# Kernel optimization log

Measured on AMD Instinct MI355X. Metric: run time of the kernel, lower is better.

Reference implementation:

```python
import jax, jax.numpy as jnp
import numpy as np

BETA = 0.25
EPS = 1e-12  # torch F.normalize eps


def _normalize(x):
    n = jnp.linalg.norm(x, axis=-1, keepdims=True)
    return x / jnp.maximum(n, EPS)


def setup_inputs() -> dict:
    key = jax.random.key(0)
    k1, k2 = jax.random.split(key)
    B, S, D, NE = 16, 2048, 512, 8192
    z = jax.random.normal(k1, (B, S, D), dtype=jnp.float32)
    emb = jax.random.normal(k2, (NE, D), dtype=jnp.float32)
    return {"z": z, "emb": emb}


def reference(z, emb):
    B, S, D = z.shape
    n_e = emb.shape[0]
    zf = z.reshape(-1, D)                      # [N, D]
    zn = _normalize(zf)
    embn = _normalize(emb)                     # [n_e, D]
    # squared euclidean distances: [N, n_e]
    d = (jnp.sum(zn * zn, axis=1, keepdims=True)
         + jnp.sum(embn * embn, axis=1)
         - 2.0 * jnp.matmul(zn, embn.T))
    idx = jnp.argmin(d, axis=1)                # [N]
    z_q = emb[idx].reshape(z.shape)            # raw codebook lookup (NOT normalized)
    # commitment / codebook loss on normalized vectors
    z_q_n = _normalize(z_q)
    z_n = _normalize(z)
    sg = jax.lax.stop_gradient
    loss = (jnp.mean((z_q_n - sg(z_n)) ** 2)
            + BETA * jnp.mean((sg(z_q_n) - z_n) ** 2))
    # straight-through estimator, then normalize
    z_q_st = z + sg(z_q - z)
    z_q_st = _normalize(z_q_st)
    # perplexity via usage counts (equivalent to mean of one-hots)
    N = zf.shape[0]
    counts = jnp.zeros((n_e,), dtype=z.dtype).at[idx].add(1.0)
    e_mean = counts / N
    perplexity = jnp.exp(-jnp.sum(e_mean * jnp.log(e_mean + 1e-10)))
    return loss, z_q_st, idx, perplexity
```

## Files before the change

### kernel.cpp

```cpp
#include <hip/hip_runtime.h>
#include <float.h>
#include <math.h>

#define DIM 512
#define EPSN 1e-12f

typedef _Float16 f16x8 __attribute__((ext_vector_type(8)));
typedef float f32x4 __attribute__((ext_vector_type(4)));

__device__ inline void gll16(const void* g, void* l) {
  __builtin_amdgcn_global_load_lds(
      (__attribute__((address_space(1))) void*)g,
      (__attribute__((address_space(3))) void*)l, 16, 0, 0);
}

__device__ inline float wave_sum(float v) {
#pragma unroll
  for (int o = 32; o > 0; o >>= 1) v += __shfl_xor(v, o, 64);
  return v;
}

__global__ __launch_bounds__(256) void emb_norm_kernel(
    const float* __restrict__ emb, float2* __restrict__ eepair) {
  int row = blockIdx.x * 4 + (threadIdx.x >> 6);
  int lane = threadIdx.x & 63;
  const float* p = emb + (size_t)row * DIM;
  float x[8];
  float ss = 0.f;
#pragma unroll
  for (int i = 0; i < 8; ++i) { x[i] = p[i * 64 + lane]; ss += x[i] * x[i]; }
  ss = wave_sum(ss);
  float d = fmaxf(sqrtf(ss), EPSN);
  float ee = 0.f;
#pragma unroll
  for (int i = 0; i < 8; ++i) { float y = x[i] / d; ee += y * y; }
  ee = wave_sum(ee);
  if (lane == 0) eepair[row] = make_float2(ee, 1.0f / d);
}

__global__ __launch_bounds__(256) void z_norm_kernel(
    const float* __restrict__ z, float* __restrict__ zinv) {
  int row = blockIdx.x * 4 + (threadIdx.x >> 6);
  int lane = threadIdx.x & 63;
  const float* p = z + (size_t)row * DIM;
  float ss = 0.f;
#pragma unroll
  for (int i = 0; i < 8; ++i) { float v = p[i * 64 + lane]; ss += v * v; }
  ss = wave_sum(ss);
  if (lane == 0) zinv[row] = 1.0f / fmaxf(sqrtf(ss), EPSN);
}

__global__ __launch_bounds__(256) void emb_split_kernel(
    const float* __restrict__ emb, const float2* __restrict__ eepair,
    _Float16* __restrict__ swz) {
  int g = blockIdx.x * 256 + threadIdx.x;
  int lane = g & 63;
  int kc = (g >> 6) & 15;
  int t = g >> 10;
  int code = t * 16 + (lane & 15);
  int k0 = kc * 32 + (lane >> 4) * 8;
  float sc = 1024.0f * eepair[code].y;
  const float* src = emb + (size_t)code * DIM + k0;
  float4 a = *(const float4*)src;
  float4 b = *(const float4*)(src + 4);
  float v[8] = {a.x, a.y, a.z, a.w, b.x, b.y, b.z, b.w};
  f16x8 h, l;
#pragma unroll
  for (int k = 0; k < 8; ++k) {
    float vs = v[k] * sc;
    _Float16 hh = (_Float16)vs;
    h[k] = hh;
    l[k] = (_Float16)(vs - (float)hh);
  }
  size_t cbase = ((size_t)(t * 16 + kc) * 2) * 512;
  *(f16x8*)&swz[cbase + lane * 8] = h;
  *(f16x8*)&swz[cbase + 512 + lane * 8] = l;
}

#define MFMA16(A, B, C) __builtin_amdgcn_mfma_f32_16x16x32_f16(A, B, C, 0, 0, 0)

__global__ __launch_bounds__(256, 1) void dist_argmin_kernel(
    const float* __restrict__ z, const _Float16* __restrict__ swz,
    int ne, int nrows, float* __restrict__ pscore, int* __restrict__ pidx) {
  __shared__ __attribute__((aligned(16))) _Float16 Bb[4][16384];

  const int tid = threadIdx.x;
  const int wave = tid >> 6;
  const int lane = tid & 63;
  const int col = lane & 15;
  const int quad = lane >> 4;
  const int part = blockIdx.x & 7;
  const int r0 = (blockIdx.x >> 3) * 128 + wave * 32;
  const int ntl = ne >> 7;
  const int tbase = part * ntl;

  f16x8 Ah[2][16], Al[2][16];
#pragma unroll
  for (int rb = 0; rb < 2; ++rb) {
    const float* zp = z + (size_t)(r0 + rb * 16 + col) * DIM + quad * 8;
#pragma unroll
    for (int kc = 0; kc < 16; ++kc) {
      float4 a = *(const float4*)(zp + kc * 32);
      float4 b = *(const float4*)(zp + kc * 32 + 4);
      float v[8] = {a.x, a.y, a.z, a.w, b.x, b.y, b.z, b.w};
#pragma unroll
      for (int k = 0; k < 8; ++k) {
        _Float16 h = (_Float16)v[k];
        Ah[rb][kc][k] = h;
        Al[rb][kc][k] = (_Float16)(v[k] - (float)h);
      }
    }
  }

  float best[2][4] = {{-FLT_MAX, -FLT_MAX, -FLT_MAX, -FLT_MAX},
                      {-FLT_MAX, -FLT_MAX, -FLT_MAX, -FLT_MAX}};
  int bidx[2][4] = {{0, 0, 0, 0}, {0, 0, 0, 0}};

  auto issue = [&](int t) {
    const int buf = t & 3;
    const _Float16* gb =
        swz + (size_t)(tbase + t) * 16384 + (wave * 8) * 512 + lane * 8;
    _Float16* lb = &Bb[buf][(wave * 8) * 512 + lane * 8];
#pragma unroll
    for (int i = 0; i < 8; ++i) gll16(gb + i * 512, lb + i * 512);
  };

  issue(0);
  issue(1);
  issue(2);

  for (int t = 0; t < ntl; ++t) {
    if (t < ntl - 2)
      asm volatile("s_waitcnt vmcnt(16)" ::: "memory");
    else if (t == ntl - 2)
      asm volatile("s_waitcnt vmcnt(8)" ::: "memory");
    else
      asm volatile("s_waitcnt vmcnt(0)" ::: "memory");
    __builtin_amdgcn_s_barrier();
    __builtin_amdgcn_sched_barrier(0);

    if (t + 3 < ntl) issue(t + 3);

    const int buf = t & 3;

    f32x4 acc[2][3];
#pragma unroll
    for (int rb = 0; rb < 2; ++rb)
#pragma unroll
      for (int a = 0; a < 3; ++a) acc[rb][a] = (f32x4){0.f, 0.f, 0.f, 0.f};

    const _Float16* bp = &Bb[buf][lane * 8];
    __builtin_amdgcn_s_setprio(1);
#pragma unroll
    for (int kc = 0; kc < 16; ++kc) {
      f16x8 bh = *(const f16x8*)(bp + (kc * 2) * 512);
      f16x8 bl = *(const f16x8*)(bp + (kc * 2 + 1) * 512);
      acc[0][0] = MFMA16(Ah[0][kc], bh, acc[0][0]);
      acc[1][0] = MFMA16(Ah[1][kc], bh, acc[1][0]);
      acc[0][1] = MFMA16(Al[0][kc], bh, acc[0][1]);
      acc[1][1] = MFMA16(Al[1][kc], bh, acc[1][1]);
      acc[0][2] = MFMA16(Ah[0][kc], bl, acc[0][2]);
      acc[1][2] = MFMA16(Ah[1][kc], bl, acc[1][2]);
    }
    __builtin_amdgcn_s_setprio(0);

    int j = (tbase + t) * 16 + col;
#pragma unroll
    for (int rb = 0; rb < 2; ++rb)
#pragma unroll
      for (int i = 0; i < 4; ++i) {
        float d = acc[rb][0][i] + acc[rb][1][i] + acc[rb][2][i];
        if (d > best[rb][i]) { best[rb][i] = d; bidx[rb][i] = j; }
      }
  }

#pragma unroll
  for (int rb = 0; rb < 2; ++rb)
#pragma unroll
    for (int i = 0; i < 4; ++i) {
      float bs = best[rb][i];
      int bj = bidx[rb][i];
#pragma unroll
      for (int offm = 1; offm < 16; offm <<= 1) {
        float os = __shfl_xor(bs, offm, 64);
        int oi = __shfl_xor(bj, offm, 64);
        if (os > bs || (os == bs && oi < bj)) { bs = os; bj = oi; }
      }
      if (col == 0) {
        int row = r0 + rb * 16 + quad * 4 + i;
        pscore[(size_t)part * nrows + row] = bs;
        pidx[(size_t)part * nrows + row] = bj;
      }
    }
}

__global__ __launch_bounds__(256) void merge_kernel(
    const float* __restrict__ pscore, const int* __restrict__ pidx,
    int nrows, int* __restrict__ idxw, float* __restrict__ counts,
    float* __restrict__ out_idx) {
  int row = blockIdx.x * 256 + threadIdx.x;
  float bs = pscore[row];
  int bj = pidx[row];
#pragma unroll
  for (int p = 1; p < 8; ++p) {
    float s = pscore[(size_t)p * nrows + row];
    int j2 = pidx[(size_t)p * nrows + row];
    if (s > bs || (s == bs && j2 < bj)) { bs = s; bj = j2; }
  }
  idxw[row] = bj;
  out_idx[row] = (float)bj;
  atomicAdd(&counts[bj], 1.0f);
}

__global__ __launch_bounds__(256) void finalize_rows_kernel(
    const float* __restrict__ z, const float* __restrict__ emb,
    const int* __restrict__ idxw, const float* __restrict__ zinv,
    float* __restrict__ out_zq, float* __restrict__ lpart) {
  __shared__ float red[4];
  int row = blockIdx.x * 4 + (threadIdx.x >> 6);
  int lane = threadIdx.x & 63;
  int j = idxw[row];
  const float* zp = z + (size_t)row * DIM;
  const float* qp = emb + (size_t)j * DIM;
  float zl[8], ql[8], tl[8];
  float st = 0.f, sq = 0.f;
#pragma unroll
  for (int i = 0; i < 8; ++i) {
    int k = i * 64 + lane;
    float zv = zp[k], qv = qp[k];
    float t = zv + (qv - zv);
    zl[i] = zv; ql[i] = qv; tl[i] = t;
    st += t * t;
    sq += qv * qv;
  }
  st = wave_sum(st);
  sq = wave_sum(sq);
  float dt = fmaxf(sqrtf(st), EPSN);
  float dq = fmaxf(sqrtf(sq), EPSN);
  float zi = zinv[row];
  float lp = 0.f;
#pragma unroll
  for (int i = 0; i < 8; ++i) {
    int k = i * 64 + lane;
    out_zq[(size_t)row * DIM + k] = tl[i] / dt;
    float e = ql[i] / dq - zl[i] * zi;
    lp += e * e;
  }
  lp = wave_sum(lp);
  if (lane == 0) red[threadIdx.x >> 6] = lp;
  __syncthreads();
  if (threadIdx.x == 0) lpart[blockIdx.x] = red[0] + red[1] + red[2] + red[3];
}

__global__ __launch_bounds__(256) void scalars_kernel(
    const float* __restrict__ counts, const float* __restrict__ lpart,
    int ne, int nblk, float inv_n, float inv_total,
    float* __restrict__ out_loss, float* __restrict__ out_perp) {
  __shared__ float red[8];
  int tid = threadIdx.x;
  float s = 0.f;
  for (int jj = tid; jj < ne; jj += 256) {
    float p = counts[jj] * inv_n;
    s += p * logf(p + 1e-10f);
  }
  float l = 0.f;
  for (int jj = tid; jj < nblk; jj += 256) l += lpart[jj];
  s = wave_sum(s);
  l = wave_sum(l);
  if ((tid & 63) == 0) { red[tid >> 6] = s; red[4 + (tid >> 6)] = l; }
  __syncthreads();
  if (tid == 0) {
    float t = red[0] + red[1] + red[2] + red[3];
    float lt = red[4] + red[5] + red[6] + red[7];
    *out_perp = expf(-t);
    *out_loss = 1.25f * lt * inv_total;
  }
}

extern "C" void kernel_launch(void* const* d_in, const int* in_sizes, int n_in,
                              void* d_out, int out_size, void* d_ws, size_t ws_size,
                              hipStream_t stream) {
  const float* z = (const float*)d_in[0];
  const float* emb = (const float*)d_in[1];
  float* out = (float*)d_out;
  float* ws = (float*)d_ws;

  const int nrows = in_sizes[0] / DIM;
  const int ne = in_sizes[1] / DIM;
  const int nfin = nrows / 4;

  float2* eepair = (float2*)ws;
  float* zinv = ws + 2 * ne;
  int* idxw = (int*)(ws + 2 * ne + nrows);
  float* counts = ws + 2 * ne + 2 * nrows;
  float* lpart = counts + ne;
  float* pscore = lpart + nfin;
  int* pidx = (int*)(pscore + 8 * (size_t)nrows);
  _Float16* swz = (_Float16*)(pidx + 8 * (size_t)nrows);

  float* out_zq = out + 1;
  float* out_idx = out + 1 + (size_t)nrows * DIM;
  float* out_perp = out + (size_t)out_size - 1;

  hipMemsetAsync(counts, 0, ne * sizeof(float), stream);
  emb_norm_kernel<<<ne / 4, 256, 0, stream>>>(emb, eepair);
  z_norm_kernel<<<nrows / 4, 256, 0, stream>>>(z, zinv);
  emb_split_kernel<<<ne * 64 / 256, 256, 0, stream>>>(emb, eepair, swz);
  dist_argmin_kernel<<<(nrows / 128) * 8, 256, 0, stream>>>(z, swz, ne, nrows,
                                                            pscore, pidx);
  merge_kernel<<<nrows / 256, 256, 0, stream>>>(pscore, pidx, nrows,
                                                idxw, counts, out_idx);
  finalize_rows_kernel<<<nfin, 256, 0, stream>>>(z, emb, idxw, zinv,
                                                 out_zq, lpart);
  scalars_kernel<<<1, 256, 0, stream>>>(counts, lpart, ne, nfin,
                                        1.0f / (float)nrows,
                                        1.0f / (float)((size_t)nrows * DIM),
                                        out, out_perp);
}
```

Before: 1.058 ms.

## Restructure argmin kernel to 8 waves with register-staged double buffering

The distance/argmin kernel moves from 4 waves each owning 32 rows to 8 waves each owning 16 rows. The 4-deep global_load_lds LDS pipeline with manual vmcnt waits is replaced by a 2-buffer scheme that stages tiles through registers and synchronises with __syncthreads. Halving per-wave A fragments and LDS use, with launch bounds (512,2), is meant to raise occupancy and latency hiding. In exchange, each B fragment read from LDS now feeds half as many MFMAs, and register staging with full barriers adds VGPR traffic and sync overhead.

```diff
diff --git a/kernel.cpp b/kernel.cpp
--- a/kernel.cpp
+++ b/kernel.cpp
@@ -7,12 +7,6 @@
 
 typedef _Float16 f16x8 __attribute__((ext_vector_type(8)));
 typedef float f32x4 __attribute__((ext_vector_type(4)));
-
-__device__ inline void gll16(const void* g, void* l) {
-  __builtin_amdgcn_global_load_lds(
-      (__attribute__((address_space(1))) void*)g,
-      (__attribute__((address_space(3))) void*)l, 16, 0, 0);
-}
 
 __device__ inline float wave_sum(float v) {
 #pragma unroll
@@ -79,10 +73,10 @@
 
 #define MFMA16(A, B, C) __builtin_amdgcn_mfma_f32_16x16x32_f16(A, B, C, 0, 0, 0)
 
-__global__ __launch_bounds__(256, 1) void dist_argmin_kernel(
+__global__ __launch_bounds__(512, 2) void dist_argmin_kernel(
     const float* __restrict__ z, const _Float16* __restrict__ swz,
     int ne, int nrows, float* __restrict__ pscore, int* __restrict__ pidx) {
-  __shared__ __attribute__((aligned(16))) _Float16 Bb[4][16384];
+  __shared__ __attribute__((aligned(16))) _Float16 Bb[2][16384];
 
   const int tid = threadIdx.x;
   const int wave = tid >> 6;
@@ -90,14 +84,32 @@
   const int col = lane & 15;
   const int quad = lane >> 4;
   const int part = blockIdx.x & 7;
-  const int r0 = (blockIdx.x >> 3) * 128 + wave * 32;
+  const int r0 = (blockIdx.x >> 3) * 128 + wave * 16;
   const int ntl = ne >> 7;
   const int tbase = part * ntl;
 
-  f16x8 Ah[2][16], Al[2][16];
-#pragma unroll
-  for (int rb = 0; rb < 2; ++rb) {
-    const float* zp = z + (size_t)(r0 + rb * 16 + col) * DIM + quad * 8;
+  float best[4] = {-FLT_MAX, -FLT_MAX, -FLT_MAX, -FLT_MAX};
+  int bidx[4] = {0, 0, 0, 0};
+
+  f16x8 R0[4], R1[4];
+  auto load_tile = [&](int t, f16x8* R) {
+    const _Float16* gb =
+        swz + (size_t)(tbase + t) * 16384 + (wave * 4) * 512 + lane * 8;
+#pragma unroll
+    for (int i = 0; i < 4; ++i) R[i] = *(const f16x8*)(gb + i * 512);
+  };
+  auto write_tile = [&](int buf, const f16x8* R) {
+    _Float16* lb = &Bb[buf][(wave * 4) * 512 + lane * 8];
+#pragma unroll
+    for (int i = 0; i < 4; ++i) *(f16x8*)(lb + i * 512) = R[i];
+  };
+
+  load_tile(0, R0);
+  load_tile(1, R1);
+
+  f16x8 Ah[16], Al[16];
+  {
+    const float* zp = z + (size_t)(r0 + col) * DIM + quad * 8;
 #pragma unroll
     for (int kc = 0; kc < 16; ++kc) {
       float4 a = *(const float4*)(zp + kc * 32);
@@ -106,92 +118,65 @@
 #pragma unroll
       for (int k = 0; k < 8; ++k) {
         _Float16 h = (_Float16)v[k];
-        Ah[rb][kc][k] = h;
-        Al[rb][kc][k] = (_Float16)(v[k] - (float)h);
+        Ah[kc][k] = h;
+        Al[kc][k] = (_Float16)(v[k] - (float)h);
       }
     }
   }
 
-  float best[2][4] = {{-FLT_MAX, -FLT_MAX, -FLT_MAX, -FLT_MAX},
-                      {-FLT_MAX, -FLT_MAX, -FLT_MAX, -FLT_MAX}};
-  int bidx[2][4] = {{0, 0, 0, 0}, {0, 0, 0, 0}};
-
-  auto issue = [&](int t) {
-    const int buf = t & 3;
-    const _Float16* gb =
-        swz + (size_t)(tbase + t) * 16384 + (wave * 8) * 512 + lane * 8;
-    _Float16* lb = &Bb[buf][(wave * 8) * 512 + lane * 8];
-#pragma unroll
-    for (int i = 0; i < 8; ++i) gll16(gb + i * 512, lb + i * 512);
-  };
-
-  issue(0);
-  issue(1);
-  issue(2);
-
-  for (int t = 0; t < ntl; ++t) {
-    if (t < ntl - 2)
-      asm volatile("s_waitcnt vmcnt(16)" ::: "memory");
-    else if (t == ntl - 2)
-      asm volatile("s_waitcnt vmcnt(8)" ::: "memory");
-    else
-      asm volatile("s_waitcnt vmcnt(0)" ::: "memory");
-    __builtin_amdgcn_s_barrier();
-    __builtin_amdgcn_sched_barrier(0);
-
-    if (t + 3 < ntl) issue(t + 3);
-
-    const int buf = t & 3;
-
-    f32x4 acc[2][3];
-#pragma unroll
-    for (int rb = 0; rb < 2; ++rb)
-#pragma unroll
-      for (int a = 0; a < 3; ++a) acc[rb][a] = (f32x4){0.f, 0.f, 0.f, 0.f};
-
+  auto compute_tile = [&](int t, int buf) {
+    f32x4 a0 = (f32x4){0.f, 0.f, 0.f, 0.f};
+    f32x4 a1 = a0, a2 = a0;
     const _Float16* bp = &Bb[buf][lane * 8];
     __builtin_amdgcn_s_setprio(1);
 #pragma unroll
     for (int kc = 0; kc < 16; ++kc) {
       f16x8 bh = *(const f16x8*)(bp + (kc * 2) * 512);
       f16x8 bl = *(const f16x8*)(bp + (kc * 2 + 1) * 512);
-      acc[0][0] = MFMA16(Ah[0][kc], bh, acc[0][0]);
-      acc[1][0] = MFMA16(Ah[1][kc], bh, acc[1][0]);
-      acc[0][1] = MFMA16(Al[0][kc], bh, acc[0][1]);
-      acc[1][1] = MFMA16(Al[1][kc], bh, acc[1][1]);
-      acc[0][2] = MFMA16(Ah[0][kc], bl, acc[0][2]);
-      acc[1][2] = MFMA16(Ah[1][kc], bl, acc[1][2]);
+      a0 = MFMA16(Ah[kc], bh, a0);
+      a1 = MFMA16(Al[kc], bh, a1);
+      a2 = MFMA16(Ah[kc], bl, a2);
     }
     __builtin_amdgcn_s_setprio(0);
-
     int j = (tbase + t) * 16 + col;
 #pragma unroll
-    for (int rb = 0; rb < 2; ++rb)
-#pragma unroll
-      for (int i = 0; i < 4; ++i) {
-        float d = acc[rb][0][i] + acc[rb][1][i] + acc[rb][2][i];
-        if (d > best[rb][i]) { best[rb][i] = d; bidx[rb][i] = j; }
-      }
-  }
-
-#pragma unroll
-  for (int rb = 0; rb < 2; ++rb)
-#pragma unroll
     for (int i = 0; i < 4; ++i) {
-      float bs = best[rb][i];
-      int bj = bidx[rb][i];
-#pragma unroll
-      for (int offm = 1; offm < 16; offm <<= 1) {
-        float os = __shfl_xor(bs, offm, 64);
-        int oi = __shfl_xor(bj, offm, 64);
-        if (os > bs || (os == bs && oi < bj)) { bs = os; bj = oi; }
-      }
-      if (col == 0) {
-        int row = r0 + rb * 16 + quad * 4 + i;
-        pscore[(size_t)part * nrows + row] = bs;
-        pidx[(size_t)part * nrows + row] = bj;
-      }
-    }
+      float d = a0[i] + a1[i] + a2[i];
+      if (d > best[i]) { best[i] = d; bidx[i] = j; }
+    }
+  };
+
+  write_tile(0, R0);
+  __syncthreads();
+
+  for (int t = 0; t < ntl; t += 2) {
+    if (t + 2 < ntl) load_tile(t + 2, R0);
+    compute_tile(t, 0);
+    write_tile(1, R1);
+    __syncthreads();
+
+    if (t + 3 < ntl) load_tile(t + 3, R1);
+    compute_tile(t + 1, 1);
+    if (t + 2 < ntl) write_tile(0, R0);
+    __syncthreads();
+  }
+
+#pragma unroll
+  for (int i = 0; i < 4; ++i) {
+    float bs = best[i];
+    int bj = bidx[i];
+#pragma unroll
+    for (int offm = 1; offm < 16; offm <<= 1) {
+      float os = __shfl_xor(bs, offm, 64);
+      int oi = __shfl_xor(bj, offm, 64);
+      if (os > bs || (os == bs && oi < bj)) { bs = os; bj = oi; }
+    }
+    if (col == 0) {
+      int row = r0 + quad * 4 + i;
+      pscore[(size_t)part * nrows + row] = bs;
+      pidx[(size_t)part * nrows + row] = bj;
+    }
+  }
 }
 
 __global__ __launch_bounds__(256) void merge_kernel(
@@ -306,7 +291,7 @@
   emb_norm_kernel<<<ne / 4, 256, 0, stream>>>(emb, eepair);
   z_norm_kernel<<<nrows / 4, 256, 0, stream>>>(z, zinv);
   emb_split_kernel<<<ne * 64 / 256, 256, 0, stream>>>(emb, eepair, swz);
-  dist_argmin_kernel<<<(nrows / 128) * 8, 256, 0, stream>>>(z, swz, ne, nrows,
+  dist_argmin_kernel<<<(nrows / 128) * 8, 512, 0, stream>>>(z, swz, ne, nrows,
                                                             pscore, pidx);
   merge_kernel<<<nrows / 256, 256, 0, stream>>>(pscore, pidx, nrows,
                                                 idxw, counts, out_idx);
```

New measurement: 900.6 us. 14.9% less time.

## Replace direct global-to-LDS loads with register-staged double-buffered prefetch

Applied to the files above, without the earlier changes.

Replaces the 4-deep async global_load_lds pipeline with loads into registers (two tile register sets), which are then written to a 2-buffer LDS ring around __syncthreads. This halves LDS usage and lets the compiler schedule ordinary vector loads, in exchange for extra VGPR pressure (16 f16x8 staging registers on top of the large A fragments) and explicit LDS stores. Prefetch depth drops from three tiles ahead to one or two tiles ahead, which may expose more memory latency.

```diff
diff --git a/kernel.cpp b/kernel.cpp
--- a/kernel.cpp
+++ b/kernel.cpp
@@ -7,12 +7,6 @@
 
 typedef _Float16 f16x8 __attribute__((ext_vector_type(8)));
 typedef float f32x4 __attribute__((ext_vector_type(4)));
-
-__device__ inline void gll16(const void* g, void* l) {
-  __builtin_amdgcn_global_load_lds(
-      (__attribute__((address_space(1))) void*)g,
-      (__attribute__((address_space(3))) void*)l, 16, 0, 0);
-}
 
 __device__ inline float wave_sum(float v) {
 #pragma unroll
@@ -82,7 +76,7 @@
 __global__ __launch_bounds__(256, 1) void dist_argmin_kernel(
     const float* __restrict__ z, const _Float16* __restrict__ swz,
     int ne, int nrows, float* __restrict__ pscore, int* __restrict__ pidx) {
-  __shared__ __attribute__((aligned(16))) _Float16 Bb[4][16384];
+  __shared__ __attribute__((aligned(16))) _Float16 Bb[2][16384];
 
   const int tid = threadIdx.x;
   const int wave = tid >> 6;
@@ -94,6 +88,26 @@
   const int ntl = ne >> 7;
   const int tbase = part * ntl;
 
+  float best[2][4] = {{-FLT_MAX, -FLT_MAX, -FLT_MAX, -FLT_MAX},
+                      {-FLT_MAX, -FLT_MAX, -FLT_MAX, -FLT_MAX}};
+  int bidx[2][4] = {{0, 0, 0, 0}, {0, 0, 0, 0}};
+
+  f16x8 R0[8], R1[8];
+  auto load_tile = [&](int t, f16x8* R) {
+    const _Float16* gb =
+        swz + (size_t)(tbase + t) * 16384 + (wave * 8) * 512 + lane * 8;
+#pragma unroll
+    for (int i = 0; i < 8; ++i) R[i] = *(const f16x8*)(gb + i * 512);
+  };
+  auto write_tile = [&](int buf, const f16x8* R) {
+    _Float16* lb = &Bb[buf][(wave * 8) * 512 + lane * 8];
+#pragma unroll
+    for (int i = 0; i < 8; ++i) *(f16x8*)(lb + i * 512) = R[i];
+  };
+
+  load_tile(0, R0);
+  load_tile(1, R1);
+
   f16x8 Ah[2][16], Al[2][16];
 #pragma unroll
   for (int rb = 0; rb < 2; ++rb) {
@@ -112,37 +126,7 @@
     }
   }
 
-  float best[2][4] = {{-FLT_MAX, -FLT_MAX, -FLT_MAX, -FLT_MAX},
-                      {-FLT_MAX, -FLT_MAX, -FLT_MAX, -FLT_MAX}};
-  int bidx[2][4] = {{0, 0, 0, 0}, {0, 0, 0, 0}};
-
-  auto issue = [&](int t) {
-    const int buf = t & 3;
-    const _Float16* gb =
-        swz + (size_t)(tbase + t) * 16384 + (wave * 8) * 512 + lane * 8;
-    _Float16* lb = &Bb[buf][(wave * 8) * 512 + lane * 8];
-#pragma unroll
-    for (int i = 0; i < 8; ++i) gll16(gb + i * 512, lb + i * 512);
-  };
-
-  issue(0);
-  issue(1);
-  issue(2);
-
-  for (int t = 0; t < ntl; ++t) {
-    if (t < ntl - 2)
-      asm volatile("s_waitcnt vmcnt(16)" ::: "memory");
-    else if (t == ntl - 2)
-      asm volatile("s_waitcnt vmcnt(8)" ::: "memory");
-    else
-      asm volatile("s_waitcnt vmcnt(0)" ::: "memory");
-    __builtin_amdgcn_s_barrier();
-    __builtin_amdgcn_sched_barrier(0);
-
-    if (t + 3 < ntl) issue(t + 3);
-
-    const int buf = t & 3;
-
+  auto compute_tile = [&](int t, int buf) {
     f32x4 acc[2][3];
 #pragma unroll
     for (int rb = 0; rb < 2; ++rb)
@@ -172,6 +156,21 @@
         float d = acc[rb][0][i] + acc[rb][1][i] + acc[rb][2][i];
         if (d > best[rb][i]) { best[rb][i] = d; bidx[rb][i] = j; }
       }
+  };
+
+  write_tile(0, R0);
+  __syncthreads();
+
+  for (int t = 0; t < ntl; t += 2) {
+    if (t + 2 < ntl) load_tile(t + 2, R0);
+    compute_tile(t, 0);
+    write_tile(1, R1);
+    __syncthreads();
+
+    if (t + 3 < ntl) load_tile(t + 3, R1);
+    compute_tile(t + 1, 1);
+    if (t + 2 < ntl) write_tile(0, R0);
+    __syncthreads();
   }
 
 #pragma unroll
```

Result: slower. 1.234 ms (+16.6%).
